# Optimization experiments

Hardware: AMD Instinct MI355X
Metric: run time of the kernel (lower is better)

The kernel has to match this reference:

```python
import jax, jax.numpy as jnp
import numpy as np

N, D_IN, HID, N_CLS, E = 100000, 256, 128, 41, 1600000


def setup_inputs() -> dict:
    key = jax.random.key(0)
    ks = jax.random.split(key, 8)
    x = jax.random.normal(ks[0], (N, D_IN), dtype=jnp.float32)
    edge_index = jax.random.randint(ks[1], (2, E), 0, N, dtype=jnp.int64)
    s = 1.0 / np.sqrt(D_IN)
    W1 = jax.random.uniform(ks[2], (D_IN, HID), jnp.float32, -s, s)
    b1 = jnp.zeros((HID,), jnp.float32)
    s2 = 1.0 / np.sqrt(HID)
    W2 = jax.random.uniform(ks[3], (HID, HID), jnp.float32, -s2, s2)
    b2 = jnp.zeros((HID,), jnp.float32)
    lin_w = jax.random.uniform(ks[4], (HID, N_CLS), jnp.float32, -s2, s2)
    lin_b = jnp.zeros((N_CLS,), jnp.float32)
    return {"x": x, "edge_index": edge_index, "W1": W1, "b1": b1,
            "W2": W2, "b2": b2, "lin_w": lin_w, "lin_b": lin_b}


def _gcn_conv(h, src, dst, norm, W, b, n):
    # h: [N, F_in]; transform then gather-scale-scatter (PyG GCNConv order)
    h = h @ W                                   # [N, F_out]
    msg = h[src] * norm[:, None]                # [E+N, F_out]
    return jax.ops.segment_sum(msg, dst, num_segments=n) + b


def reference(x, edge_index, W1, b1, W2, b2, lin_w, lin_b):
    n = x.shape[0]
    loops = jnp.arange(n, dtype=edge_index.dtype)
    src = jnp.concatenate([edge_index[0], loops])  # add self-loops
    dst = jnp.concatenate([edge_index[1], loops])
    # symmetric normalization D^-1/2 (A+I) D^-1/2
    deg = jax.ops.segment_sum(jnp.ones_like(dst, dtype=x.dtype), dst, num_segments=n)
    dis = jnp.where(deg > 0, jax.lax.rsqrt(jnp.maximum(deg, 1.0)), 0.0)
    norm = dis[src] * dis[dst]                   # [E+N]

    x1 = jax.nn.relu(_gcn_conv(x, src, dst, norm, W1, b1, n))   # dropout is identity in eval
    x2 = jax.nn.relu(_gcn_conv(x1, src, dst, norm, W2, b2, n))
    out = (x1 + x2) @ lin_w + lin_b
    return jax.nn.log_softmax(out, axis=1)
```

## Files before the change

### kernel.cpp

```cpp
#include <hip/hip_runtime.h>
#include <math.h>


#define NPAD (1 << 17)
#define CHUNK 1024

typedef __attribute__((ext_vector_type(8))) short short8;
typedef __attribute__((ext_vector_type(4))) float f32x4;

__device__ inline unsigned short f2bf(float f) {
    unsigned u = __builtin_bit_cast(unsigned, f);
    return (unsigned short)((u + 0x7fffu + ((u >> 16) & 1u)) >> 16);
}
__device__ inline float bflo(unsigned u) { return __builtin_bit_cast(float, u << 16); }
__device__ inline float bfhi(unsigned u) { return __builtin_bit_cast(float, u & 0xffff0000u); }


__global__ void hist_kernel(const int* __restrict__ dst, int* __restrict__ cnt, int E) {
    int e = blockIdx.x * 256 + threadIdx.x;
    if (e < E) atomicAdd(&cnt[dst[e]], 1);
}

__global__ void scan_partial(const int* __restrict__ cnt, int* __restrict__ partial, int n) {
    __shared__ int sdata[4];
    int b = blockIdx.x, t = threadIdx.x;
    int base = b * CHUNK;
    int sum = 0;
    for (int i = t; i < CHUNK; i += 256) {
        int idx = base + i;
        if (idx < n) sum += cnt[idx];
    }
#pragma unroll
    for (int off = 32; off > 0; off >>= 1) sum += __shfl_down(sum, off, 64);
    if ((t & 63) == 0) sdata[t >> 6] = sum;
    __syncthreads();
    if (t == 0) partial[b] = sdata[0] + sdata[1] + sdata[2] + sdata[3];
}

__global__ void scan_small(int* partial, int nblk) {
    if (threadIdx.x == 0 && blockIdx.x == 0) {
        int acc = 0;
        for (int i = 0; i < nblk; i++) { int v = partial[i]; partial[i] = acc; acc += v; }
    }
}

__global__ void scan_final(const int* __restrict__ cnt, const int* __restrict__ partial,
                           int* __restrict__ offs, int* __restrict__ cursor,
                           float* __restrict__ dis, int n) {
    __shared__ int wsum[4];
    int b = blockIdx.x, t = threadIdx.x;
    int lane = t & 63, w = t >> 6;
    int base = b * CHUNK + t * 4;
    int v[4];
#pragma unroll
    for (int j = 0; j < 4; j++) v[j] = (base + j < n) ? cnt[base + j] : 0;
    int s4 = v[0] + v[1] + v[2] + v[3];
    int inc = s4;
#pragma unroll
    for (int off = 1; off < 64; off <<= 1) {
        int x = __shfl_up(inc, off, 64);
        if (lane >= off) inc += x;
    }
    if (lane == 63) wsum[w] = inc;
    __syncthreads();
    int woff = 0;
    for (int i = 0; i < 4; i++) if (i < w) woff += wsum[i];
    int pos = partial[b] + woff + (inc - s4);
#pragma unroll
    for (int j = 0; j < 4; j++) {
        int idx = base + j;
        if (idx < n) {
            offs[idx] = pos;
            cursor[idx] = pos;
            dis[idx] = rsqrtf((float)(v[j] + 1));
            pos += v[j];
        }
    }
}

__global__ void permute_bucket(const int* __restrict__ src, const int* __restrict__ dst,
                               const float* __restrict__ dis,
                               int* __restrict__ cursor, int2* __restrict__ eadj,
                               int E, int lo, int hi) {
    int e = blockIdx.x * 256 + threadIdx.x;
    if (e < E) {
        int d = dst[e];
        if (d >= lo && d < hi) {
            int s = src[e];
            int pos = atomicAdd(&cursor[d], 1);
            float wt = dis[s] * dis[d];
            eadj[pos] = make_int2(s, __float_as_int(wt));
        }
    }
}

__global__ void wcast(const float* __restrict__ W, unsigned short* __restrict__ Wt, int K) {
    int i = blockIdx.x * 256 + threadIdx.x;
    if (i < K * 128) {
        int k = i >> 7, nn = i & 127;
        Wt[nn * K + k] = f2bf(W[i]);
    }
}

template<bool ABF16>
__global__ __launch_bounds__(256) void gemm_mfma(const void* __restrict__ Ap,
                                                 const unsigned short* __restrict__ Wt,
                                                 unsigned short* __restrict__ Hb,
                                                 int n, int K) {
    __shared__ unsigned short bs[128 * 136];
    const int tid = threadIdx.x;
    const int wave = tid >> 6, lane = tid & 63;
    const int quad = lane >> 4, mrow = lane & 15;
    const int arow_g = blockIdx.x * 64 + wave * 16 + mrow;
    const int arow = arow_g < n ? arow_g : n - 1;

    f32x4 acc[8];
#pragma unroll
    for (int t = 0; t < 8; t++) acc[t] = (f32x4){0.f, 0.f, 0.f, 0.f};

    const float* Af = (const float*)Ap;
    const unsigned short* Ab = (const unsigned short*)Ap;

    for (int kc = 0; kc < K; kc += 128) {
        __syncthreads();
        for (int i = tid; i < 2048; i += 256) {
            int row = i >> 4, c8 = i & 15;
            *(short8*)&bs[row * 136 + c8 * 8] = *(const short8*)&Wt[row * K + kc + c8 * 8];
        }
        __syncthreads();
#pragma unroll
        for (int kt = 0; kt < 128; kt += 32) {
            union { short8 v; unsigned short u[8]; } A;
            if (ABF16) {
                A.v = *(const short8*)&Ab[(size_t)arow * K + kc + kt + quad * 8];
            } else {
                const float* ap = &Af[(size_t)arow * K + kc + kt + quad * 8];
                float4 p0 = *(const float4*)ap;
                float4 p1 = *(const float4*)(ap + 4);
                A.u[0] = f2bf(p0.x); A.u[1] = f2bf(p0.y);
                A.u[2] = f2bf(p0.z); A.u[3] = f2bf(p0.w);
                A.u[4] = f2bf(p1.x); A.u[5] = f2bf(p1.y);
                A.u[6] = f2bf(p1.z); A.u[7] = f2bf(p1.w);
            }
#pragma unroll
            for (int nt = 0; nt < 8; nt++) {
                short8 B = *(const short8*)&bs[(nt * 16 + mrow) * 136 + kt + quad * 8];
                acc[nt] = __builtin_amdgcn_mfma_f32_16x16x32_bf16(A.v, B, acc[nt], 0, 0, 0);
            }
        }
    }
    const int drow0 = blockIdx.x * 64 + wave * 16 + quad * 4;
#pragma unroll
    for (int r = 0; r < 4; r++) {
        int dr = drow0 + r;
        if (dr < n) {
#pragma unroll
            for (int nt = 0; nt < 8; nt++)
                Hb[(size_t)dr * 128 + nt * 16 + mrow] = f2bf(acc[nt][r]);
        }
    }
}

template<bool FUSE>
__global__ __launch_bounds__(256) void gather_k(const unsigned short* __restrict__ Hb,
                                                const int2* __restrict__ eadj,
                                                const int* __restrict__ offs,
                                                const int* __restrict__ cnt,
                                                const float* __restrict__ dis,
                                                const float* __restrict__ bias,
                                                unsigned short* __restrict__ outb,
                                                const unsigned short* __restrict__ x1b,
                                                const float* __restrict__ lw,
                                                const float* __restrict__ lb,
                                                float* __restrict__ out, int n) {
    __shared__ float s[4][128];
    const int w = threadIdx.x >> 6, lane = threadIdx.x & 63;
    const int grp = lane >> 4, fl = lane & 15;
    const int node = blockIdx.x * 4 + w;
    const int nd = node < n ? node : n - 1;
    const int st = offs[nd], c = cnt[nd];
    const unsigned short* Hfl = Hb + fl * 8;

    float acc[8];
#pragma unroll
    for (int k = 0; k < 8; k++) acc[k] = 0.f;

    const int2* ep = eadj + st;
    for (int kk = 0; kk < c; kk += 64) {
        int li = kk + lane;
        int2 me = ep[li < c ? li : c - 1];
        float mw = li < c ? __int_as_float(me.y) : 0.f;
        int cend = (c - kk) < 64 ? (c - kk) : 64;

        int   s0 = __shfl(me.x, grp, 64);
        float w0 = __shfl(mw,  grp, 64);
        int   s1 = __shfl(me.x, 4 + grp, 64);
        float w1 = __shfl(mw,  4 + grp, 64);
        uint4 r0 = *(const uint4*)(Hfl + (size_t)s0 * 128);
        uint4 r1 = *(const uint4*)(Hfl + (size_t)s1 * 128);

        for (int j = 0; j < cend; j += 8) {
            int jn = (j + 8 < cend) ? j + 8 : j;
            int   sn0 = __shfl(me.x, jn + grp, 64);
            float wn0 = __shfl(mw,  jn + grp, 64);
            int   sn1 = __shfl(me.x, jn + 4 + grp, 64);
            float wn1 = __shfl(mw,  jn + 4 + grp, 64);
            uint4 rn0 = *(const uint4*)(Hfl + (size_t)sn0 * 128);
            uint4 rn1 = *(const uint4*)(Hfl + (size_t)sn1 * 128);
            acc[0] = fmaf(bflo(r0.x), w0, acc[0]); acc[1] = fmaf(bfhi(r0.x), w0, acc[1]);
            acc[2] = fmaf(bflo(r0.y), w0, acc[2]); acc[3] = fmaf(bfhi(r0.y), w0, acc[3]);
            acc[4] = fmaf(bflo(r0.z), w0, acc[4]); acc[5] = fmaf(bfhi(r0.z), w0, acc[5]);
            acc[6] = fmaf(bflo(r0.w), w0, acc[6]); acc[7] = fmaf(bfhi(r0.w), w0, acc[7]);
            acc[0] = fmaf(bflo(r1.x), w1, acc[0]); acc[1] = fmaf(bfhi(r1.x), w1, acc[1]);
            acc[2] = fmaf(bflo(r1.y), w1, acc[2]); acc[3] = fmaf(bfhi(r1.y), w1, acc[3]);
            acc[4] = fmaf(bflo(r1.z), w1, acc[4]); acc[5] = fmaf(bfhi(r1.z), w1, acc[5]);
            acc[6] = fmaf(bflo(r1.w), w1, acc[6]); acc[7] = fmaf(bfhi(r1.w), w1, acc[7]);
            r0 = rn0; r1 = rn1; w0 = wn0; w1 = wn1;
        }
    }
#pragma unroll
    for (int k = 0; k < 8; k++) {
        acc[k] += __shfl_xor(acc[k], 16, 64);
        acc[k] += __shfl_xor(acc[k], 32, 64);
    }
    float dd = dis[nd], sn = dd * dd;
    uint4 rs = *(const uint4*)(Hfl + (size_t)nd * 128);
    float4 bb0 = ((const float4*)bias)[fl * 2];
    float4 bb1 = ((const float4*)bias)[fl * 2 + 1];
    acc[0] = fmaf(bflo(rs.x), sn, acc[0]) + bb0.x;
    acc[1] = fmaf(bfhi(rs.x), sn, acc[1]) + bb0.y;
    acc[2] = fmaf(bflo(rs.y), sn, acc[2]) + bb0.z;
    acc[3] = fmaf(bfhi(rs.y), sn, acc[3]) + bb0.w;
    acc[4] = fmaf(bflo(rs.z), sn, acc[4]) + bb1.x;
    acc[5] = fmaf(bfhi(rs.z), sn, acc[5]) + bb1.y;
    acc[6] = fmaf(bflo(rs.w), sn, acc[6]) + bb1.z;
    acc[7] = fmaf(bfhi(rs.w), sn, acc[7]) + bb1.w;
#pragma unroll
    for (int k = 0; k < 8; k++) acc[k] = acc[k] > 0.f ? acc[k] : 0.f;

    if (!FUSE) {
        if (node < n && grp == 0) {
            uint4 pk;
            pk.x = ((unsigned)f2bf(acc[1]) << 16) | (unsigned)f2bf(acc[0]);
            pk.y = ((unsigned)f2bf(acc[3]) << 16) | (unsigned)f2bf(acc[2]);
            pk.z = ((unsigned)f2bf(acc[5]) << 16) | (unsigned)f2bf(acc[4]);
            pk.w = ((unsigned)f2bf(acc[7]) << 16) | (unsigned)f2bf(acc[6]);
            *(uint4*)(outb + (size_t)node * 128 + fl * 8) = pk;
        }
    } else {
        if (grp == 0) {
            uint4 xv = *(const uint4*)(x1b + (size_t)nd * 128 + fl * 8);
            s[w][fl * 8 + 0] = acc[0] + bflo(xv.x);
            s[w][fl * 8 + 1] = acc[1] + bfhi(xv.x);
            s[w][fl * 8 + 2] = acc[2] + bflo(xv.y);
            s[w][fl * 8 + 3] = acc[3] + bfhi(xv.y);
            s[w][fl * 8 + 4] = acc[4] + bflo(xv.z);
            s[w][fl * 8 + 5] = acc[5] + bfhi(xv.z);
            s[w][fl * 8 + 6] = acc[6] + bflo(xv.w);
            s[w][fl * 8 + 7] = acc[7] + bfhi(xv.w);
        }
        __syncthreads();
        bool act = (node < n) && (lane < 41);
        float val = 0.f;
        if (act) {
#pragma unroll 4
            for (int f = 0; f < 128; f++) val = fmaf(s[w][f], lw[f * 41 + lane], val);
            val += lb[lane];
        }
        float m = act ? val : -INFINITY;
#pragma unroll
        for (int off = 32; off > 0; off >>= 1) m = fmaxf(m, __shfl_xor(m, off, 64));
        float e = act ? expf(val - m) : 0.f;
#pragma unroll
        for (int off = 32; off > 0; off >>= 1) e += __shfl_xor(e, off, 64);
        if (act) out[(size_t)node * 41 + lane] = val - m - logf(e);
    }
}

extern "C" void kernel_launch(void* const* d_in, const int* in_sizes, int n_in,
                              void* d_out, int out_size, void* d_ws, size_t ws_size,
                              hipStream_t stream) {
    const float* x  = (const float*)d_in[0];
    const int*   ei = (const int*)d_in[1];
    const float* W1 = (const float*)d_in[2];
    const float* b1 = (const float*)d_in[3];
    const float* W2 = (const float*)d_in[4];
    const float* b2 = (const float*)d_in[5];
    const float* lw = (const float*)d_in[6];
    const float* lb = (const float*)d_in[7];
    float* out = (float*)d_out;

    const int n = in_sizes[0] / 256;
    const int E = in_sizes[1] / 2;
    const int* src = ei;
    const int* dst = ei + E;

    int*   cnt     = (int*)d_ws;
    int*   offs    = cnt + NPAD;
    int*   cursor  = offs + NPAD;
    int*   partial = cursor + NPAD;
    float* dis     = (float*)(partial + 1024);
    size_t Epad    = ((size_t)E + 255) & ~(size_t)255;
    int2*  eadj    = (int2*)(dis + NPAD);
    unsigned short* Wt1 = (unsigned short*)(eadj + Epad);
    unsigned short* Wt2 = Wt1 + 256 * 128;
    unsigned short* Hb  = Wt2 + 128 * 128;
    unsigned short* X1b = Hb + (size_t)n * 128;

    const int nscan = (n + CHUNK - 1) / CHUNK;

    hipMemsetAsync(cnt, 0, (size_t)n * sizeof(int), stream);
    wcast<<<(256 * 128 + 255) / 256, 256, 0, stream>>>(W1, Wt1, 256);
    wcast<<<(128 * 128 + 255) / 256, 256, 0, stream>>>(W2, Wt2, 128);

    hist_kernel<<<(E + 255) / 256, 256, 0, stream>>>(dst, cnt, E);
    scan_partial<<<nscan, 256, 0, stream>>>(cnt, partial, n);
    scan_small<<<1, 64, 0, stream>>>(partial, nscan);
    scan_final<<<nscan, 256, 0, stream>>>(cnt, partial, offs, cursor, dis, n);
    {
        const int NBUCKET = 2;
        int W = (n + NBUCKET - 1) / NBUCKET;
        for (int p = 0; p < NBUCKET; p++) {
            int lo = p * W, hi = lo + W < n ? lo + W : n;
            permute_bucket<<<(E + 255) / 256, 256, 0, stream>>>(src, dst, dis, cursor, eadj, E, lo, hi);
        }
    }

    gemm_mfma<false><<<(n + 63) / 64, 256, 0, stream>>>(x, Wt1, Hb, n, 256);
    gather_k<false><<<(n + 3) / 4, 256, 0, stream>>>(Hb, eadj, offs, cnt, dis, b1, X1b,
                                                     nullptr, nullptr, nullptr, nullptr, n);

    gemm_mfma<true><<<(n + 63) / 64, 256, 0, stream>>>(X1b, Wt2, Hb, n, 128);
    gather_k<true><<<(n + 3) / 4, 256, 0, stream>>>(Hb, eadj, offs, cnt, dis, b2, nullptr,
                                                    X1b, lw, lb, out, n);
}
```

Baseline: 603.3 us.

## Bucket edge permutation by source, deepen gather prefetch, use packed FMA

The permute pass now buckets edges by source node instead of destination and uses 8 buckets instead of 2. Within each CSR segment, edges then come out grouped by source range, which should improve locality of the later row gathers. The gather kernel now prefetches 16 edges per step instead of 8, uses packed 2-wide FMAs for the bf16 accumulation, and sets an occupancy hint of 6 blocks per CU. In exchange, the permute kernel reads the edge list 8 times, and the deeper prefetch raises register pressure.

```diff
diff --git a/kernel.cpp b/kernel.cpp
--- a/kernel.cpp
+++ b/kernel.cpp
@@ -7,6 +7,7 @@
 
 typedef __attribute__((ext_vector_type(8))) short short8;
 typedef __attribute__((ext_vector_type(4))) float f32x4;
+typedef __attribute__((ext_vector_type(2))) float f32x2;
 
 __device__ inline unsigned short f2bf(float f) {
     unsigned u = __builtin_bit_cast(unsigned, f);
@@ -14,6 +15,9 @@
 }
 __device__ inline float bflo(unsigned u) { return __builtin_bit_cast(float, u << 16); }
 __device__ inline float bfhi(unsigned u) { return __builtin_bit_cast(float, u & 0xffff0000u); }
+__device__ inline f32x2 up2(unsigned u) {
+    f32x2 r; r.x = bflo(u); r.y = bfhi(u); return r;
+}
 
 
 __global__ void hist_kernel(const int* __restrict__ dst, int* __restrict__ cnt, int E) {
@@ -84,9 +88,9 @@
                                int E, int lo, int hi) {
     int e = blockIdx.x * 256 + threadIdx.x;
     if (e < E) {
-        int d = dst[e];
-        if (d >= lo && d < hi) {
-            int s = src[e];
+        int s = src[e];
+        if (s >= lo && s < hi) {
+            int d = dst[e];
             int pos = atomicAdd(&cursor[d], 1);
             float wt = dis[s] * dis[d];
             eadj[pos] = make_int2(s, __float_as_int(wt));
@@ -161,8 +165,32 @@
     }
 }
 
+
+#define STAGE(R0, R1, R2, R3, W0, W1, W2, W3, J) {                 \
+    int _s0 = __shfl(me.x, (J) + grp, 64);                         \
+    W0 = __shfl(mw, (J) + grp, 64);                                \
+    int _s1 = __shfl(me.x, (J) + 4 + grp, 64);                     \
+    W1 = __shfl(mw, (J) + 4 + grp, 64);                            \
+    int _s2 = __shfl(me.x, (J) + 8 + grp, 64);                     \
+    W2 = __shfl(mw, (J) + 8 + grp, 64);                            \
+    int _s3 = __shfl(me.x, (J) + 12 + grp, 64);                    \
+    W3 = __shfl(mw, (J) + 12 + grp, 64);                           \
+    R0 = *(const uint4*)(Hfl + (size_t)_s0 * 128);                 \
+    R1 = *(const uint4*)(Hfl + (size_t)_s1 * 128);                 \
+    R2 = *(const uint4*)(Hfl + (size_t)_s2 * 128);                 \
+    R3 = *(const uint4*)(Hfl + (size_t)_s3 * 128);                 \
+}
+
+#define CONS1(R, W) {                                              \
+    f32x2 _w = (f32x2){(W), (W)};                                  \
+    a0 = __builtin_elementwise_fma(up2(R.x), _w, a0);              \
+    a1 = __builtin_elementwise_fma(up2(R.y), _w, a1);              \
+    a2 = __builtin_elementwise_fma(up2(R.z), _w, a2);              \
+    a3 = __builtin_elementwise_fma(up2(R.w), _w, a3);              \
+}
+
 template<bool FUSE>
-__global__ __launch_bounds__(256) void gather_k(const unsigned short* __restrict__ Hb,
+__global__ __launch_bounds__(256, 6) void gather_k(const unsigned short* __restrict__ Hb,
                                                 const int2* __restrict__ eadj,
                                                 const int* __restrict__ offs,
                                                 const int* __restrict__ cnt,
@@ -181,9 +209,8 @@
     const int st = offs[nd], c = cnt[nd];
     const unsigned short* Hfl = Hb + fl * 8;
 
-    float acc[8];
-#pragma unroll
-    for (int k = 0; k < 8; k++) acc[k] = 0.f;
+    f32x2 a0 = (f32x2){0.f, 0.f}, a1 = (f32x2){0.f, 0.f};
+    f32x2 a2 = (f32x2){0.f, 0.f}, a3 = (f32x2){0.f, 0.f};
 
     const int2* ep = eadj + st;
     for (int kk = 0; kk < c; kk += 64) {
@@ -192,72 +219,72 @@
         float mw = li < c ? __int_as_float(me.y) : 0.f;
         int cend = (c - kk) < 64 ? (c - kk) : 64;
 
-        int   s0 = __shfl(me.x, grp, 64);
-        float w0 = __shfl(mw,  grp, 64);
-        int   s1 = __shfl(me.x, 4 + grp, 64);
-        float w1 = __shfl(mw,  4 + grp, 64);
-        uint4 r0 = *(const uint4*)(Hfl + (size_t)s0 * 128);
-        uint4 r1 = *(const uint4*)(Hfl + (size_t)s1 * 128);
-
-        for (int j = 0; j < cend; j += 8) {
-            int jn = (j + 8 < cend) ? j + 8 : j;
-            int   sn0 = __shfl(me.x, jn + grp, 64);
-            float wn0 = __shfl(mw,  jn + grp, 64);
-            int   sn1 = __shfl(me.x, jn + 4 + grp, 64);
-            float wn1 = __shfl(mw,  jn + 4 + grp, 64);
-            uint4 rn0 = *(const uint4*)(Hfl + (size_t)sn0 * 128);
-            uint4 rn1 = *(const uint4*)(Hfl + (size_t)sn1 * 128);
-            acc[0] = fmaf(bflo(r0.x), w0, acc[0]); acc[1] = fmaf(bfhi(r0.x), w0, acc[1]);
-            acc[2] = fmaf(bflo(r0.y), w0, acc[2]); acc[3] = fmaf(bfhi(r0.y), w0, acc[3]);
-            acc[4] = fmaf(bflo(r0.z), w0, acc[4]); acc[5] = fmaf(bfhi(r0.z), w0, acc[5]);
-            acc[6] = fmaf(bflo(r0.w), w0, acc[6]); acc[7] = fmaf(bfhi(r0.w), w0, acc[7]);
-            acc[0] = fmaf(bflo(r1.x), w1, acc[0]); acc[1] = fmaf(bfhi(r1.x), w1, acc[1]);
-            acc[2] = fmaf(bflo(r1.y), w1, acc[2]); acc[3] = fmaf(bfhi(r1.y), w1, acc[3]);
-            acc[4] = fmaf(bflo(r1.z), w1, acc[4]); acc[5] = fmaf(bfhi(r1.z), w1, acc[5]);
-            acc[6] = fmaf(bflo(r1.w), w1, acc[6]); acc[7] = fmaf(bfhi(r1.w), w1, acc[7]);
-            r0 = rn0; r1 = rn1; w0 = wn0; w1 = wn1;
-        }
-    }
-#pragma unroll
-    for (int k = 0; k < 8; k++) {
-        acc[k] += __shfl_xor(acc[k], 16, 64);
-        acc[k] += __shfl_xor(acc[k], 32, 64);
-    }
+        uint4 r0, r1, r2, r3;
+        float w0, w1, w2, w3;
+        STAGE(r0, r1, r2, r3, w0, w1, w2, w3, 0);
+        int j = 0;
+        while (true) {
+            int jn = j + 16;
+            if (jn < cend) {
+                uint4 n0, n1, n2, n3;
+                float v0, v1, v2, v3;
+                STAGE(n0, n1, n2, n3, v0, v1, v2, v3, jn);
+                CONS1(r0, w0); CONS1(r1, w1); CONS1(r2, w2); CONS1(r3, w3);
+                r0 = n0; r1 = n1; r2 = n2; r3 = n3;
+                w0 = v0; w1 = v1; w2 = v2; w3 = v3;
+                j = jn;
+            } else {
+                CONS1(r0, w0); CONS1(r1, w1); CONS1(r2, w2); CONS1(r3, w3);
+                break;
+            }
+        }
+    }
+    a0.x += __shfl_xor(a0.x, 16, 64); a0.x += __shfl_xor(a0.x, 32, 64);
+    a0.y += __shfl_xor(a0.y, 16, 64); a0.y += __shfl_xor(a0.y, 32, 64);
+    a1.x += __shfl_xor(a1.x, 16, 64); a1.x += __shfl_xor(a1.x, 32, 64);
+    a1.y += __shfl_xor(a1.y, 16, 64); a1.y += __shfl_xor(a1.y, 32, 64);
+    a2.x += __shfl_xor(a2.x, 16, 64); a2.x += __shfl_xor(a2.x, 32, 64);
+    a2.y += __shfl_xor(a2.y, 16, 64); a2.y += __shfl_xor(a2.y, 32, 64);
+    a3.x += __shfl_xor(a3.x, 16, 64); a3.x += __shfl_xor(a3.x, 32, 64);
+    a3.y += __shfl_xor(a3.y, 16, 64); a3.y += __shfl_xor(a3.y, 32, 64);
+
     float dd = dis[nd], sn = dd * dd;
     uint4 rs = *(const uint4*)(Hfl + (size_t)nd * 128);
     float4 bb0 = ((const float4*)bias)[fl * 2];
     float4 bb1 = ((const float4*)bias)[fl * 2 + 1];
-    acc[0] = fmaf(bflo(rs.x), sn, acc[0]) + bb0.x;
-    acc[1] = fmaf(bfhi(rs.x), sn, acc[1]) + bb0.y;
-    acc[2] = fmaf(bflo(rs.y), sn, acc[2]) + bb0.z;
-    acc[3] = fmaf(bfhi(rs.y), sn, acc[3]) + bb0.w;
-    acc[4] = fmaf(bflo(rs.z), sn, acc[4]) + bb1.x;
-    acc[5] = fmaf(bfhi(rs.z), sn, acc[5]) + bb1.y;
-    acc[6] = fmaf(bflo(rs.w), sn, acc[6]) + bb1.z;
-    acc[7] = fmaf(bfhi(rs.w), sn, acc[7]) + bb1.w;
-#pragma unroll
-    for (int k = 0; k < 8; k++) acc[k] = acc[k] > 0.f ? acc[k] : 0.f;
+    a0.x = fmaf(bflo(rs.x), sn, a0.x) + bb0.x;
+    a0.y = fmaf(bfhi(rs.x), sn, a0.y) + bb0.y;
+    a1.x = fmaf(bflo(rs.y), sn, a1.x) + bb0.z;
+    a1.y = fmaf(bfhi(rs.y), sn, a1.y) + bb0.w;
+    a2.x = fmaf(bflo(rs.z), sn, a2.x) + bb1.x;
+    a2.y = fmaf(bfhi(rs.z), sn, a2.y) + bb1.y;
+    a3.x = fmaf(bflo(rs.w), sn, a3.x) + bb1.z;
+    a3.y = fmaf(bfhi(rs.w), sn, a3.y) + bb1.w;
+    a0.x = a0.x > 0.f ? a0.x : 0.f;  a0.y = a0.y > 0.f ? a0.y : 0.f;
+    a1.x = a1.x > 0.f ? a1.x : 0.f;  a1.y = a1.y > 0.f ? a1.y : 0.f;
+    a2.x = a2.x > 0.f ? a2.x : 0.f;  a2.y = a2.y > 0.f ? a2.y : 0.f;
+    a3.x = a3.x > 0.f ? a3.x : 0.f;  a3.y = a3.y > 0.f ? a3.y : 0.f;
 
     if (!FUSE) {
         if (node < n && grp == 0) {
             uint4 pk;
-            pk.x = ((unsigned)f2bf(acc[1]) << 16) | (unsigned)f2bf(acc[0]);
-            pk.y = ((unsigned)f2bf(acc[3]) << 16) | (unsigned)f2bf(acc[2]);
-            pk.z = ((unsigned)f2bf(acc[5]) << 16) | (unsigned)f2bf(acc[4]);
-            pk.w = ((unsigned)f2bf(acc[7]) << 16) | (unsigned)f2bf(acc[6]);
+            pk.x = ((unsigned)f2bf(a0.y) << 16) | (unsigned)f2bf(a0.x);
+            pk.y = ((unsigned)f2bf(a1.y) << 16) | (unsigned)f2bf(a1.x);
+            pk.z = ((unsigned)f2bf(a2.y) << 16) | (unsigned)f2bf(a2.x);
+            pk.w = ((unsigned)f2bf(a3.y) << 16) | (unsigned)f2bf(a3.x);
             *(uint4*)(outb + (size_t)node * 128 + fl * 8) = pk;
         }
     } else {
         if (grp == 0) {
             uint4 xv = *(const uint4*)(x1b + (size_t)nd * 128 + fl * 8);
-            s[w][fl * 8 + 0] = acc[0] + bflo(xv.x);
-            s[w][fl * 8 + 1] = acc[1] + bfhi(xv.x);
-            s[w][fl * 8 + 2] = acc[2] + bflo(xv.y);
-            s[w][fl * 8 + 3] = acc[3] + bfhi(xv.y);
-            s[w][fl * 8 + 4] = acc[4] + bflo(xv.z);
-            s[w][fl * 8 + 5] = acc[5] + bfhi(xv.z);
-            s[w][fl * 8 + 6] = acc[6] + bflo(xv.w);
-            s[w][fl * 8 + 7] = acc[7] + bfhi(xv.w);
+            s[w][fl * 8 + 0] = a0.x + bflo(xv.x);
+            s[w][fl * 8 + 1] = a0.y + bfhi(xv.x);
+            s[w][fl * 8 + 2] = a1.x + bflo(xv.y);
+            s[w][fl * 8 + 3] = a1.y + bfhi(xv.y);
+            s[w][fl * 8 + 4] = a2.x + bflo(xv.z);
+            s[w][fl * 8 + 5] = a2.y + bfhi(xv.z);
+            s[w][fl * 8 + 6] = a3.x + bflo(xv.w);
+            s[w][fl * 8 + 7] = a3.y + bfhi(xv.w);
         }
         __syncthreads();
         bool act = (node < n) && (lane < 41);
@@ -318,7 +345,7 @@
     scan_small<<<1, 64, 0, stream>>>(partial, nscan);
     scan_final<<<nscan, 256, 0, stream>>>(cnt, partial, offs, cursor, dis, n);
     {
-        const int NBUCKET = 2;
+        const int NBUCKET = 8;
         int W = (n + NBUCKET - 1) / NBUCKET;
         for (int p = 0; p < NBUCKET; p++) {
             int lo = p * W, hi = lo + W < n ? lo + W : n;
```

New measurement: 646.5 us. 1.07x slower.
